# Kernel tuning notes

Measured on AMD Instinct MI355X. Metric: run time of the kernel, lower is better.

## Reference

```python
import jax, jax.numpy as jnp
import numpy as np
from jax import lax

NUM_GROUP = 128   # G
GROUP_SIZE = 32   # S
ENC = 384         # encoder_channel
BN_EPS = 1e-5


def fps(pos, K):
    # farthest point sampling; deterministic start at index 0. pos: [B,N,3] -> idx [B,K]
    B, N, _ = pos.shape
    d0 = jnp.full((B, N), jnp.inf, pos.dtype)
    start = jnp.zeros((B,), jnp.int32)

    def step(carry, _):
        d, last = carry
        p = jnp.take_along_axis(pos, last[:, None, None], axis=1)  # [B,1,3]
        dist = jnp.sum((pos - p) ** 2, -1)
        d = jnp.minimum(d, dist)
        nxt = jnp.argmax(d, axis=1).astype(jnp.int32)
        return (d, nxt), last

    _, idxs = lax.scan(step, (d0, start), None, length=K)  # [K,B]
    return jnp.transpose(idxs)


def knn_idx(q, t, k):
    # squared euclidean distances, k smallest (sorted ascending)
    d2 = (jnp.sum(q * q, -1)[:, :, None] + jnp.sum(t * t, -1)[:, None, :]
          - 2.0 * jnp.einsum('bqc,bnc->bqn', q, t))
    _, idx = lax.top_k(-d2, k)
    return idx


def gather_nn(x, idx):
    # x: [B,N,C], idx: [B,...] -> [B,...,C]
    return jax.vmap(lambda a, i: a[i])(x, idx)


def disambiguate(lps, vecs):
    # lps: [B,G,S,3], vecs: [B,G,3]; flip vec if it points away from the majority of points
    S = lps.shape[2]
    proj = jnp.einsum('bgc,bgsc->bgs', vecs, lps)
    n_pos = jnp.sum((proj > 0).astype(jnp.float32), axis=2, keepdims=True)
    flip = (n_pos < 0.5 * S).astype(jnp.float32)
    return (1.0 - 2.0 * flip) * vecs


def bn(x, g, b):
    # eval-mode BatchNorm with running_mean=0, running_var=1
    return x * (g / jnp.sqrt(1.0 + BN_EPS)) + b


def forward(pc, W1, b1, g1, be1, W2, b2, W3, b3, g2, be2, W4, b4):
    # ---- Group: FPS + KNN gather ----
    rep = fps(pc, NUM_GROUP)                      # [B,G]
    center = gather_nn(pc, rep)                   # [B,G,3]
    nn = knn_idx(center, pc, GROUP_SIZE)          # [B,G,S]
    neigh = gather_nn(pc, nn) - center[:, :, None]  # [B,G,S,3] centered local sets
    # ---- LRF: weighted PCA via 3x3 eigensolve ----
    norms = jnp.linalg.norm(neigh, axis=3, keepdims=True)
    w = jnp.max(norms, axis=2, keepdims=True) - norms
    w = w / (jnp.sum(w, axis=2, keepdims=True) + 1e-6)
    sp = 100.0 * neigh
    covs = jnp.einsum('bgsk,bgsl->bgkl', w * sp, sp)  # [B,G,3,3]
    _, eigvec = jnp.linalg.eigh(covs)                 # eigenvalues ascending
    z = disambiguate(neigh, eigvec[..., 0])           # smallest-eig axis
    x_ax = disambiguate(neigh, eigvec[..., 2])        # largest-eig axis
    y = jnp.cross(z, x_ax)
    lrfs = jnp.stack((z, y, x_ax), axis=3)            # [B,G,3,3] columns z,y,x
    rot = jnp.einsum('bgsc,bgcd->bgsd', neigh, lrfs)  # rotation-normalized points
    # ---- LocalPointSetEncoder: kernel-1 convs as matmuls ----
    f = jnp.einsum('bgsc,oc->bgso', rot, W1) + b1     # [B,G,S,128]
    f = jax.nn.relu(bn(f, g1, be1))
    f = jnp.einsum('bgso,po->bgsp', f, W2) + b2       # [B,G,S,256]
    fg = jnp.max(f, axis=2, keepdims=True)            # [B,G,1,256]
    f = jnp.concatenate([jnp.broadcast_to(fg, f.shape), f], axis=-1)  # [B,G,S,512]
    f = jnp.einsum('bgsc,oc->bgso', f, W3) + b3       # [B,G,S,512]
    f = jax.nn.relu(bn(f, g2, be2))
    f = jnp.einsum('bgso,po->bgsp', f, W4) + b4       # [B,G,S,ENC]
    return jnp.max(f, axis=2)                          # [B,G,ENC]


def setup_inputs() -> dict:
    key = jax.random.key(0)
    ks = jax.random.split(key, 6)
    B, N = 32, 8192
    w = lambda k, shape: (jax.random.normal(k, shape, jnp.float32) * 0.05)
    return {
        'pc': jax.random.normal(ks[0], (B, N, 3), jnp.float32),
        'W1': w(ks[1], (128, 3)), 'b1': jnp.zeros((128,), jnp.float32),
        'g1': jnp.ones((128,), jnp.float32), 'be1': jnp.zeros((128,), jnp.float32),
        'W2': w(ks[2], (256, 128)), 'b2': jnp.zeros((256,), jnp.float32),
        'W3': w(ks[3], (512, 512)), 'b3': jnp.zeros((512,), jnp.float32),
        'g2': jnp.ones((512,), jnp.float32), 'be2': jnp.zeros((512,), jnp.float32),
        'W4': w(ks[4], (ENC, 512)), 'b4': jnp.zeros((ENC,), jnp.float32),
    }


def reference(pc, W1, b1, g1, be1, W2, b2, W3, b3, g2, be2, W4, b4):
    return forward(pc, W1, b1, g1, be1, W2, b2, W3, b3, g2, be2, W4, b4)
```

## Files before the change

### kernel.cpp

```cpp
#include <hip/hip_runtime.h>
#include <math.h>

#define B_ 32
#define N_ 8192
#define G_ 128
#define S_ 32
#define ENC_ 384

typedef __attribute__((ext_vector_type(8))) short short8;
typedef __attribute__((ext_vector_type(4))) float f32x4;
typedef __attribute__((ext_vector_type(2))) unsigned u32x2;

__device__ __forceinline__ unsigned short f2bf(float x) {
  unsigned u = __float_as_uint(x);
  u = u + 0x7fffu + ((u >> 16) & 1u);
  return (unsigned short)(u >> 16);
}

__device__ __forceinline__ unsigned pk_bf16(float a, float b) {
  unsigned r;
  asm("v_cvt_pk_bf16_f32 %0, %1, %2" : "=v"(r) : "v"(a), "v"(b));
  return r;
}

template <int CTRL, int RM>
__device__ __forceinline__ unsigned long long dpp_max_rm(unsigned long long k) {
  const int lo = (int)(unsigned)k, hi = (int)(unsigned)(k >> 32);
  const int olo = __builtin_amdgcn_update_dpp(0, lo, CTRL, RM, 0xF, true);
  const int ohi = __builtin_amdgcn_update_dpp(0, hi, CTRL, RM, 0xF, true);
  const unsigned long long o =
      ((unsigned long long)(unsigned)ohi << 32) | (unsigned)(unsigned)olo;
  return o > k ? o : k;
}

template <int CTRL>
__device__ __forceinline__ float dpp_fmax(float v) {
  const int x = __builtin_amdgcn_update_dpp(0, __float_as_int(v), CTRL, 0xF, 0xF, true);
  return fmaxf(v, __int_as_float(x));
}
__device__ __forceinline__ float rowmax16(float v) {
  v = dpp_fmax<0x128>(v);
  v = dpp_fmax<0x124>(v);
  v = dpp_fmax<0x122>(v);
  v = dpp_fmax<0x121>(v);
  return v;
}

__global__ __launch_bounds__(512) void fps_kernel(const float* __restrict__ pc,
                                                  int* __restrict__ rep) {
  #pragma clang fp contract(off)
  extern __shared__ char smraw[];
  unsigned long long (*redbuf)[8] = (unsigned long long (*)[8])smraw;
  float* sx = (float*)(smraw + 128);
  float* sy = sx + N_;
  float* sz = sy + N_;
  const int b = blockIdx.x;
  const float* p = pc + (size_t)b * N_ * 3;
  const int tid = threadIdx.x;
  for (int i = tid; i < N_; i += 512) {
    sx[i] = p[i * 3 + 0];
    sy[i] = p[i * 3 + 1];
    sz[i] = p[i * 3 + 2];
  }
  __syncthreads();
  float X[16], Y[16], Z[16], D[16];
  #pragma unroll
  for (int j = 0; j < 16; ++j) {
    const int idx = tid + j * 512;
    X[j] = sx[idx]; Y[j] = sy[idx]; Z[j] = sz[idx];
    D[j] = INFINITY;
  }
  int last = 0;
  const int lane = tid & 63, wave = tid >> 6;
  for (int k = 0; k < G_; ++k) {
    if (tid == 0) rep[b * G_ + k] = last;
    const float px = sx[last], py = sy[last], pz = sz[last];
    float bestv = -1.0f;
    int besti = 0;
    #pragma unroll
    for (int j = 0; j < 16; ++j) {
      const float dx = X[j] - px, dy = Y[j] - py, dz = Z[j] - pz;
      float dist = dx * dx;
      dist += dy * dy;
      dist += dz * dz;
      const float dj = fminf(D[j], dist);
      D[j] = dj;
      if (dj > bestv) { bestv = dj; besti = tid + j * 512; }
    }
    unsigned long long key =
        ((unsigned long long)__float_as_uint(bestv) << 32) | (unsigned)(8191 - besti);
    key = dpp_max_rm<0xB1, 0xF>(key);
    key = dpp_max_rm<0x4E, 0xF>(key);
    key = dpp_max_rm<0x141, 0xF>(key);
    key = dpp_max_rm<0x140, 0xF>(key);
    key = dpp_max_rm<0x142, 0xA>(key);
    key = dpp_max_rm<0x143, 0xC>(key);
    const int par = k & 1;
    if (lane == 63) redbuf[par][wave] = key;
    __syncthreads();
    unsigned long long kk = redbuf[par][0];
    #pragma unroll
    for (int w = 1; w < 8; ++w) {
      const unsigned long long o = redbuf[par][w];
      if (o > kk) kk = o;
    }
    last = 8191 - (int)(kk & 0xFFFFFFFFu);
  }
}

__global__ __launch_bounds__(256) void knn_kernel(const float* __restrict__ pc,
                                                  const int* __restrict__ rep,
                                                  int* __restrict__ nn) {
  #pragma clang fp contract(off)
  const int bg = blockIdx.x;
  const int b = bg >> 7;
  const float* p = pc + (size_t)b * N_ * 3;
  const int tid = threadIdx.x;
  const int lane = tid & 63, wave = tid >> 6;
  const int ridx = rep[bg];
  const float qx = p[ridx * 3 + 0], qy = p[ridx * 3 + 1], qz = p[ridx * 3 + 2];
  float nq = qx * qx;
  nq += qy * qy;
  nq += qz * qz;
  unsigned ub[32];
  #pragma unroll
  for (int j = 0; j < 32; ++j) {
    const int idx = tid + j * 256;
    const float tx = p[idx * 3 + 0], ty = p[idx * 3 + 1], tz = p[idx * 3 + 2];
    float nt = tx * tx;
    nt += ty * ty;
    nt += tz * tz;
    float dt = qx * tx;
    dt += qy * ty;
    dt += qz * tz;
    const float d2 = (nq + nt) - 2.0f * dt;
    unsigned u = __float_as_uint(d2);
    u = (u & 0x80000000u) ? ~u : (u | 0x80000000u);
    ub[j] = u;
  }

  __shared__ unsigned hist[256];
  __shared__ unsigned wsum[4];
  __shared__ int s_bin, s_cexc, s_hbin, s_cnt;
  __shared__ unsigned long long keys[32];

  unsigned long long curPrefix = 0;
  int need = 32;
  int prevShift = 45;
  int stopShift = 0;
  unsigned long long stopPrefix = 0;
  const int shifts[6] = {37, 29, 21, 13, 5, 0};
  #pragma unroll 1
  for (int pass = 0; pass < 6; ++pass) {
    const int sh = shifts[pass];
    const int width = prevShift - sh;
    const unsigned msk = (1u << width) - 1u;
    hist[tid] = 0;
    if (pass == 0 && tid == 0) s_cnt = 0;
    __syncthreads();
    #pragma unroll
    for (int j = 0; j < 32; ++j) {
      const unsigned long long key =
          ((unsigned long long)ub[j] << 13) | (unsigned)(tid + j * 256);
      if ((key >> prevShift) == curPrefix)
        atomicAdd(&hist[(unsigned)(key >> sh) & msk], 1u);
    }
    __syncthreads();
    const unsigned v = hist[tid];
    unsigned c = v;
    #pragma unroll
    for (int off = 1; off <= 32; off <<= 1) {
      const unsigned o = __shfl_up(c, (unsigned)off);
      if (lane >= off) c += o;
    }
    if (lane == 63) wsum[wave] = c;
    __syncthreads();
    unsigned pre = 0;
    if (wave > 0) pre += wsum[0];
    if (wave > 1) pre += wsum[1];
    if (wave > 2) pre += wsum[2];
    const unsigned cine = c + pre;
    const unsigned cexc = cine - v;
    if (cexc < (unsigned)need && (unsigned)need <= cine) {
      s_bin = tid;
      s_cexc = (int)cexc;
      s_hbin = (int)v;
    }
    __syncthreads();
    curPrefix = (curPrefix << width) | (unsigned)s_bin;
    need -= s_cexc;
    prevShift = sh;
    if (need == s_hbin) {
      stopShift = sh;
      stopPrefix = curPrefix;
      break;
    }
  }
  #pragma unroll
  for (int j = 0; j < 32; ++j) {
    const unsigned long long key =
        ((unsigned long long)ub[j] << 13) | (unsigned)(tid + j * 256);
    if ((key >> stopShift) <= stopPrefix) {
      const int pos = atomicAdd(&s_cnt, 1);
      keys[pos] = key;
    }
  }
  __syncthreads();
  if (tid < 32) {
    const unsigned long long kt = keys[tid];
    int rank = 0;
    #pragma unroll
    for (int j = 0; j < 32; ++j) rank += (keys[j] < kt) ? 1 : 0;
    nn[bg * S_ + rank] = (int)(kt & 8191u);
  }
}

__device__ __forceinline__ double slapy2d(double x, double y) {
  return sqrt(x * x + y * y);
}

__device__ void slartg_(double f, double g, double& c, double& s, double& r) {
  if (g == 0.0) { c = 1.0; s = 0.0; r = f; }
  else if (f == 0.0) { c = 0.0; s = copysign(1.0, g); r = fabs(g); }
  else {
    const double d = sqrt(f * f + g * g);
    c = fabs(f) / d;
    r = copysign(d, f);
    s = g / r;
  }
}

__device__ void slaev2_(double a, double b, double c, double& rt1, double& rt2,
                        double& cs1, double& sn1) {
  const double sm = a + c, df = a - c;
  const double adf = fabs(df), tb = b + b, ab = fabs(tb);
  double acmx, acmn;
  if (fabs(a) > fabs(c)) { acmx = a; acmn = c; } else { acmx = c; acmn = a; }
  double rt;
  if (adf > ab) rt = adf * sqrt(1.0 + (ab / adf) * (ab / adf));
  else if (adf < ab) rt = ab * sqrt(1.0 + (adf / ab) * (adf / ab));
  else rt = ab * sqrt(2.0);
  int sgn1;
  if (sm < 0.0) { rt1 = 0.5 * (sm - rt); sgn1 = -1; rt2 = (acmx / rt1) * acmn - (b / rt1) * b; }
  else if (sm > 0.0) { rt1 = 0.5 * (sm + rt); sgn1 = 1; rt2 = (acmx / rt1) * acmn - (b / rt1) * b; }
  else { rt1 = 0.5 * rt; rt2 = -0.5 * rt; sgn1 = 1; }
  double cs;
  int sgn2;
  if (df >= 0.0) { cs = df + rt; sgn2 = 1; } else { cs = df - rt; sgn2 = -1; }
  const double acs = fabs(cs);
  if (acs > ab) {
    const double ct = -tb / cs;
    sn1 = 1.0 / sqrt(1.0 + ct * ct);
    cs1 = ct * sn1;
  } else {
    if (ab == 0.0) { cs1 = 1.0; sn1 = 0.0; }
    else {
      const double tn = -cs / tb;
      cs1 = 1.0 / sqrt(1.0 + tn * tn);
      sn1 = tn * cs1;
    }
  }
  if (sgn1 == sgn2) { const double tn = cs1; cs1 = -sn1; sn1 = tn; }
}

__device__ void eigh33_lapack(const double A[3][3], double dout[3], double Zo[3][3]) {
  double d[3], e[2];
  double Z[3][3];
  {
    const double a00 = A[0][0], a10 = A[1][0], a20 = A[2][0];
    const double a11 = A[1][1], a21 = A[2][1], a22 = A[2][2];
    if (fabs(a20) == 0.0) {
      d[0] = a00; d[1] = a11; d[2] = a22; e[0] = a10; e[1] = a21;
      Z[0][0] = 1; Z[0][1] = 0; Z[0][2] = 0;
      Z[1][0] = 0; Z[1][1] = 1; Z[1][2] = 0;
      Z[2][0] = 0; Z[2][1] = 0; Z[2][2] = 1;
    } else {
      const double beta = -copysign(slapy2d(a10, a20), a10);
      const double tau = (beta - a10) / beta;
      const double v2 = a20 / (a10 - beta);
      const double h11 = 1.0 - tau;
      const double h12 = -tau * v2;
      const double h22 = 1.0 - tau * v2 * v2;
      const double m10 = h11 * a10 + h12 * a20;
      const double m11 = h11 * a11 + h12 * a21;
      const double m12 = h11 * a21 + h12 * a22;
      const double m21 = h12 * a11 + h22 * a21;
      const double m22 = h12 * a21 + h22 * a22;
      d[0] = a00;
      d[1] = m11 * h11 + m12 * h12;
      d[2] = m21 * h12 + m22 * h22;
      e[0] = m10;
      e[1] = m21 * h11 + m22 * h12;
      Z[0][0] = 1; Z[0][1] = 0;   Z[0][2] = 0;
      Z[1][0] = 0; Z[1][1] = h11; Z[1][2] = h12;
      Z[2][0] = 0; Z[2][1] = h12; Z[2][2] = h22;
    }
  }
  const double eps = 5.9604644775390625e-08;
  const double eps2 = eps * eps;
  const double safmin = 1.1754943508222875e-38;
  int jtot = 0;
  const int nmaxit = 90;
  int l1 = 0;
  while (l1 <= 2) {
    if (l1 > 0) e[l1 - 1] = 0.0;
    int m;
    for (m = l1; m <= 1; ++m) {
      const double tst = fabs(e[m]);
      if (tst == 0.0) break;
      if (tst <= (sqrt(fabs(d[m])) * sqrt(fabs(d[m + 1]))) * eps) { e[m] = 0.0; break; }
    }
    int l = l1;
    const int lsv = l;
    int lend = m;
    const int lendsv = lend;
    l1 = m + 1;
    if (lend == l) continue;
    if (fabs(d[lend]) < fabs(d[l])) { lend = lsv; l = lendsv; }
    if (lend > l) {
      for (;;) {
        int mq;
        for (mq = l; mq <= lend - 1; ++mq) {
          const double tst = e[mq] * e[mq];
          if (tst <= (eps2 * fabs(d[mq])) * fabs(d[mq + 1]) + safmin) break;
        }
        if (mq < lend) e[mq] = 0.0;
        double p = d[l];
        if (mq == l) { d[l] = p; l = l + 1; if (l <= lend) continue; break; }
        if (mq == l + 1) {
          double rt1, rt2, c, s;
          slaev2_(d[l], e[l], d[l + 1], rt1, rt2, c, s);
          for (int i = 0; i < 3; ++i) {
            const double t1 = Z[i][l + 1], t0 = Z[i][l];
            Z[i][l + 1] = c * t1 - s * t0;
            Z[i][l] = s * t1 + c * t0;
          }
          d[l] = rt1; d[l + 1] = rt2; e[l] = 0.0;
          l += 2;
          if (l <= lend) continue;
          break;
        }
        if (jtot == nmaxit) break;
        ++jtot;
        double g = (d[l + 1] - p) / (2.0 * e[l]);
        double r = slapy2d(g, 1.0);
        g = d[mq] - p + e[l] / (g + copysign(r, g));
        double s = 1.0, c = 1.0;
        p = 0.0;
        double csv[2], ssv[2];
        for (int i = mq - 1; i >= l; --i) {
          const double f = s * e[i];
          const double bb = c * e[i];
          slartg_(g, f, c, s, r);
          if (i != mq - 1) e[i + 1] = r;
          g = d[i + 1] - p;
          r = (d[i] - g) * s + 2.0 * c * bb;
          p = s * r;
          d[i + 1] = g + p;
          g = c * r - bb;
          csv[i] = c; ssv[i] = -s;
        }
        const int mm = mq - l + 1;
        for (int j = mm - 2; j >= 0; --j) {
          const double ct = csv[l + j], st = ssv[l + j];
          for (int i = 0; i < 3; ++i) {
            const double t1 = Z[i][l + j + 1];
            Z[i][l + j + 1] = ct * t1 - st * Z[i][l + j];
            Z[i][l + j] = st * t1 + ct * Z[i][l + j];
          }
        }
        d[l] = d[l] - p;
        e[l] = g;
      }
    } else {
      for (;;) {
        int mq;
        for (mq = l; mq >= lend + 1; --mq) {
          const double tst = e[mq - 1] * e[mq - 1];
          if (tst <= (eps2 * fabs(d[mq])) * fabs(d[mq - 1]) + safmin) break;
        }
        if (mq > lend) e[mq - 1] = 0.0;
        double p = d[l];
        if (mq == l) { d[l] = p; l = l - 1; if (l >= lend) continue; break; }
        if (mq == l - 1) {
          double rt1, rt2, c, s;
          slaev2_(d[l - 1], e[l - 1], d[l], rt1, rt2, c, s);
          for (int i = 0; i < 3; ++i) {
            const double t1 = Z[i][l], t0 = Z[i][l - 1];
            Z[i][l] = c * t1 - s * t0;
            Z[i][l - 1] = s * t1 + c * t0;
          }
          d[l - 1] = rt1; d[l] = rt2; e[l - 1] = 0.0;
          l -= 2;
          if (l >= lend) continue;
          break;
        }
        if (jtot == nmaxit) break;
        ++jtot;
        double g = (d[l - 1] - p) / (2.0 * e[l - 1]);
        double r = slapy2d(g, 1.0);
        g = d[mq] - p + e[l - 1] / (g + copysign(r, g));
        double s = 1.0, c = 1.0;
        p = 0.0;
        double csv[2], ssv[2];
        for (int i = mq; i <= l - 1; ++i) {
          const double f = s * e[i];
          const double bb = c * e[i];
          slartg_(g, f, c, s, r);
          if (i != mq) e[i - 1] = r;
          g = d[i] - p;
          r = (d[i + 1] - g) * s + 2.0 * c * bb;
          p = s * r;
          d[i] = g + p;
          g = c * r - bb;
          csv[i] = c; ssv[i] = s;
        }
        const int mm = l - mq + 1;
        for (int j = 0; j <= mm - 2; ++j) {
          const double ct = csv[mq + j], st = ssv[mq + j];
          for (int i = 0; i < 3; ++i) {
            const double t1 = Z[i][mq + j + 1];
            Z[i][mq + j + 1] = ct * t1 - st * Z[i][mq + j];
            Z[i][mq + j] = st * t1 + ct * Z[i][mq + j];
          }
        }
        d[l] = d[l] - p;
        e[l - 1] = g;
      }
    }
  }
  for (int ii = 1; ii < 3; ++ii) {
    const int i = ii - 1;
    int k = i;
    double p = d[i];
    for (int j = ii; j < 3; ++j)
      if (d[j] < p) { k = j; p = d[j]; }
    if (k != i) {
      d[k] = d[i];
      d[i] = p;
      for (int q = 0; q < 3; ++q) {
        const double t = Z[q][i];
        Z[q][i] = Z[q][k];
        Z[q][k] = t;
      }
    }
  }
  dout[0] = d[0]; dout[1] = d[1]; dout[2] = d[2];
  for (int i = 0; i < 3; ++i)
    for (int j = 0; j < 3; ++j) Zo[i][j] = Z[i][j];
}

__global__ __launch_bounds__(64) void lrf_kernel(const float* __restrict__ pc,
                                                 const int* __restrict__ rep,
                                                 const int* __restrict__ nn,
                                                 float* __restrict__ rot) {
  #pragma clang fp contract(off)
  const int bg = blockIdx.x;
  const int b = bg >> 7;
  const float* p = pc + (size_t)b * N_ * 3;
  const int lane = threadIdx.x;
  const int s = lane & 31;
  const int ridx = rep[bg];
  const float cx = p[ridx * 3 + 0], cy = p[ridx * 3 + 1], cz = p[ridx * 3 + 2];
  const int idx = nn[bg * S_ + s];
  const float nx = p[idx * 3 + 0] - cx;
  const float ny = p[idx * 3 + 1] - cy;
  const float nz = p[idx * 3 + 2] - cz;
  float nrm2 = nx * nx;
  nrm2 += ny * ny;
  nrm2 += nz * nz;
  const float nrm = sqrtf(nrm2);
  float wmax = nrm;
  #pragma unroll
  for (int off = 16; off >= 1; off >>= 1) wmax = fmaxf(wmax, __shfl_xor(wmax, off));
  float w = wmax - nrm;
  float wsum = w;
  #pragma unroll
  for (int off = 16; off >= 1; off >>= 1) wsum += __shfl_xor(wsum, off);
  w = w / (wsum + 1e-6f);
  const float spx = 100.0f * nx, spy = 100.0f * ny, spz = 100.0f * nz;
  const float wx = w * spx, wy = w * spy, wz = w * spz;
  float c00 = wx * spx, c01 = wx * spy, c02 = wx * spz;
  float c11 = wy * spy, c12 = wy * spz, c22 = wz * spz;
  #pragma unroll
  for (int off = 16; off >= 1; off >>= 1) {
    c00 += __shfl_xor(c00, off); c01 += __shfl_xor(c01, off); c02 += __shfl_xor(c02, off);
    c11 += __shfl_xor(c11, off); c12 += __shfl_xor(c12, off); c22 += __shfl_xor(c22, off);
  }
  double A[3][3] = {{(double)c00, (double)c01, (double)c02},
                    {(double)c01, (double)c11, (double)c12},
                    {(double)c02, (double)c12, (double)c22}};
  double lam[3], Zm[3][3];
  eigh33_lapack(A, lam, Zm);
  float zx = (float)Zm[0][0], zy = (float)Zm[1][0], zz = (float)Zm[2][0];
  float xx = (float)Zm[0][2], xy = (float)Zm[1][2], xz = (float)Zm[2][2];
  float pj = zx * nx;
  pj += zy * ny;
  pj += zz * nz;
  int npos = __popcll(__ballot(pj > 0.0f) & 0xFFFFFFFFull);
  if (npos < 16) { zx = -zx; zy = -zy; zz = -zz; }
  pj = xx * nx;
  pj += xy * ny;
  pj += xz * nz;
  npos = __popcll(__ballot(pj > 0.0f) & 0xFFFFFFFFull);
  if (npos < 16) { xx = -xx; xy = -xy; xz = -xz; }
  const float yx = zy * xz - zz * xy;
  const float yy = zz * xx - zx * xz;
  const float yz = zx * xy - zy * xx;
  if (lane < 32) {
    float r0 = nx * zx; r0 += ny * zy; r0 += nz * zz;
    float r1 = nx * yx; r1 += ny * yy; r1 += nz * yz;
    float r2 = nx * xx; r2 += ny * xy; r2 += nz * xz;
    const size_t base = (size_t)(bg * S_ + s) * 3;
    rot[base + 0] = r0;
    rot[base + 1] = r1;
    rot[base + 2] = r2;
  }
}

#define P2_ 4096
#define P3_ 16384
#define P4_ 24576
__global__ __launch_bounds__(256) void convw_kernel(
    const float* __restrict__ W2, const float* __restrict__ W3,
    const float* __restrict__ W4, short* __restrict__ w2t,
    short* __restrict__ w3gt, short* __restrict__ w3ft,
    short* __restrict__ w4t) {
  int t = blockIdx.x * 256 + threadIdx.x;
  const float* src;
  short* dst;
  if (t < P2_) {
    const int lane = t & 63, kt = (t >> 6) & 3, nt = t >> 8;
    src = W2 + (nt * 16 + (lane & 15)) * 128 + kt * 32 + ((lane >> 4) << 3);
    dst = w2t + t * 8;
  } else if (t < P2_ + P3_) {
    const int p = t - P2_;
    const int lane = p & 63, kt = (p >> 6) & 7, nt = p >> 9;
    src = W3 + (nt * 16 + (lane & 15)) * 512 + kt * 32 + ((lane >> 4) << 3);
    dst = w3gt + p * 8;
  } else if (t < P2_ + 2 * P3_) {
    const int p = t - P2_ - P3_;
    const int lane = p & 63, kt = (p >> 6) & 7, nt = p >> 9;
    src = W3 + (nt * 16 + (lane & 15)) * 512 + 256 + kt * 32 + ((lane >> 4) << 3);
    dst = w3ft + p * 8;
  } else if (t < P2_ + 2 * P3_ + P4_) {
    const int p = t - P2_ - 2 * P3_;
    const int lane = p & 63, kt = (p >> 6) & 15, nt = p >> 10;
    src = W4 + (nt * 16 + (lane & 15)) * 512 + kt * 32 + ((lane >> 4) << 3);
    dst = w4t + p * 8;
  } else {
    return;
  }
  short8 v;
  #pragma unroll
  for (int j = 0; j < 8; ++j) v[j] = (short)f2bf(src[j]);
  *(short8*)dst = v;
}

#define OFF_A3   0
#define OFF_R1   32768
#define OFF_FGA  65536
#define OFF_BASE 73728
#define OFF_SROT 77824
#define LDS_MLP  78592

__device__ __forceinline__ int swz(int row, int byteoff) {
  return byteoff ^ ((row & 7) << 4);
}

__global__ __launch_bounds__(512) void mlp_kernel(
    const float* __restrict__ rot,
    const float* __restrict__ W1, const float* __restrict__ b1,
    const float* __restrict__ g1, const float* __restrict__ be1,
    const float* __restrict__ b2, const float* __restrict__ b3,
    const float* __restrict__ g2, const float* __restrict__ be2,
    const float* __restrict__ b4,
    const short* __restrict__ w2t, const short* __restrict__ w3gt,
    const short* __restrict__ w3ft, const short* __restrict__ w4t,
    float* __restrict__ out) {
  extern __shared__ char sm[];
  const int tid = threadIdx.x;
  const int lane = tid & 63, wave = tid >> 6;
  const int l15 = lane & 15, lq = lane >> 4;
  const int bg0 = blockIdx.x * 2;
  const float inv_s = 1.0f / sqrtf(1.0f + 1e-5f);

  if (tid < 192) ((float*)(sm + OFF_SROT))[tid] = rot[(size_t)bg0 * 96 + tid];
  for (int i = tid; i < 2048; i += 512) ((int*)(sm + OFF_FGA))[i] = 0;
  __syncthreads();

  {
    const int o2 = (tid & 63) * 2;
    const int rbase = tid >> 6;
    const float w00 = W1[o2 * 3], w01 = W1[o2 * 3 + 1], w02 = W1[o2 * 3 + 2];
    const float w10 = W1[o2 * 3 + 3], w11 = W1[o2 * 3 + 4], w12 = W1[o2 * 3 + 5];
    const float b10 = b1[o2], b11 = b1[o2 + 1];
    const float sc0 = g1[o2] * inv_s, sc1 = g1[o2 + 1] * inv_s;
    const float sh0 = be1[o2], sh1 = be1[o2 + 1];
    const float* sr = (const float*)(sm + OFF_SROT);
    #pragma unroll
    for (int t = 0; t < 8; ++t) {
      const int row = rbase + t * 8;
      const float x = sr[row * 3], y = sr[row * 3 + 1], z = sr[row * 3 + 2];
      const float v0 = fmaxf((x * w00 + y * w01 + z * w02 + b10) * sc0 + sh0, 0.0f);
      const float v1 = fmaxf((x * w10 + y * w11 + z * w12 + b11) * sc1 + sh1, 0.0f);
      *(unsigned*)(sm + OFF_R1 + swz(row, row * 256 + o2 * 2)) = pk_bf16(v0, v1);
    }
  }
  __syncthreads();

  {
    f32x4 acc[2][4];
    #pragma unroll
    for (int j = 0; j < 2; ++j)
      #pragma unroll
      for (int st = 0; st < 4; ++st) acc[j][st] = (f32x4){0.f, 0.f, 0.f, 0.f};
    #pragma unroll 1
    for (int kt = 0; kt < 4; ++kt) {
      short8 bf[4];
      #pragma unroll
      for (int st = 0; st < 4; ++st) {
        const int s = st * 16 + l15;
        bf[st] = *(const short8*)(sm + OFF_R1 + swz(s, s * 256 + kt * 64 + (lq << 4)));
      }
      #pragma unroll
      for (int j = 0; j < 2; ++j) {
        const short8 wa = *(const short8*)(w2t + (((wave * 2 + j) * 4 + kt) * 64 + lane) * 8);
        #pragma unroll
        for (int st = 0; st < 4; ++st)
          acc[j][st] = __builtin_amdgcn_mfma_f32_16x16x32_bf16(wa, bf[st], acc[j][st], 0, 0, 0);
      }
    }
    #pragma unroll
    for (int j = 0; j < 2; ++j) {
      const int n0 = (wave * 2 + j) * 16 + (lq << 2);
      const f32x4 b2v = *(const f32x4*)(b2 + n0);
      float vv[4][4];
      #pragma unroll
      for (int st = 0; st < 4; ++st) {
        #pragma unroll
        for (int r = 0; r < 4; ++r) vv[st][r] = acc[j][st][r] + b2v[r];
        const int s = st * 16 + l15;
        const unsigned lo = pk_bf16(vv[st][0], vv[st][1]);
        const unsigned hi = pk_bf16(vv[st][2], vv[st][3]);
        *(u32x2*)(sm + OFF_A3 + swz(s, s * 512 + n0 * 2)) = (u32x2){lo, hi};
      }
      float fg0[4], fg1[4];
      #pragma unroll
      for (int r = 0; r < 4; ++r) {
        fg0[r] = rowmax16(fmaxf(vv[0][r], vv[1][r]));
        fg1[r] = rowmax16(fmaxf(vv[2][r], vv[3][r]));
      }
      if (l15 == 0) {
        *(u32x2*)(sm + OFF_FGA + swz(0, n0 * 2)) =
            (u32x2){pk_bf16(fg0[0], fg0[1]), pk_bf16(fg0[2], fg0[3])};
      } else if (l15 == 1) {
        *(u32x2*)(sm + OFF_FGA + swz(1, 512 + n0 * 2)) =
            (u32x2){pk_bf16(fg1[0], fg1[1]), pk_bf16(fg1[2], fg1[3])};
      }
    }
  }
  __syncthreads();

  {
    f32x4 acg[4];
    #pragma unroll
    for (int q = 0; q < 4; ++q) acg[q] = (f32x4){0.f, 0.f, 0.f, 0.f};
    #pragma unroll 1
    for (int kt = 0; kt < 8; ++kt) {
      const short8 bf = *(const short8*)(sm + OFF_FGA + swz(l15, l15 * 512 + kt * 64 + (lq << 4)));
      #pragma unroll
      for (int q = 0; q < 4; ++q) {
        const short8 wa = *(const short8*)(w3gt + (((wave * 4 + q) * 8 + kt) * 64 + lane) * 8);
        acg[q] = __builtin_amdgcn_mfma_f32_16x16x32_bf16(wa, bf, acg[q], 0, 0, 0);
      }
    }
    if (l15 < 2) {
      #pragma unroll
      for (int q = 0; q < 4; ++q) {
        const int n3 = (wave * 4 + q) * 16 + (lq << 2);
        const f32x4 b3v = *(const f32x4*)(b3 + n3);
        *(f32x4*)(sm + OFF_BASE + l15 * 2048 + n3 * 4) = acg[q] + b3v;
      }
    }
  }
  __syncthreads();

  f32x4 acc4[3][4];
  #pragma unroll
  for (int q = 0; q < 3; ++q)
    #pragma unroll
    for (int st = 0; st < 4; ++st) acc4[q][st] = (f32x4){0.f, 0.f, 0.f, 0.f};

  #pragma unroll 1
  for (int p = 0; p < 2; ++p) {
    {
      f32x4 ac[2][4];
      #pragma unroll
      for (int jj = 0; jj < 2; ++jj)
        #pragma unroll
        for (int st = 0; st < 4; ++st) ac[jj][st] = (f32x4){0.f, 0.f, 0.f, 0.f};
      #pragma unroll 1
      for (int kt = 0; kt < 8; ++kt) {
        short8 bf[4];
        #pragma unroll
        for (int st = 0; st < 4; ++st) {
          const int s = st * 16 + l15;
          bf[st] = *(const short8*)(sm + OFF_A3 + swz(s, s * 512 + kt * 64 + (lq << 4)));
        }
        #pragma unroll
        for (int jj = 0; jj < 2; ++jj) {
          const int mt = p * 16 + wave * 2 + jj;
          const short8 wa = *(const short8*)(w3ft + ((mt * 8 + kt) * 64 + lane) * 8);
          #pragma unroll
          for (int st = 0; st < 4; ++st)
            ac[jj][st] = __builtin_amdgcn_mfma_f32_16x16x32_bf16(wa, bf[st], ac[jj][st], 0, 0, 0);
        }
      }
      #pragma unroll
      for (int jj = 0; jj < 2; ++jj) {
        const int ng = (p * 16 + wave * 2 + jj) * 16 + (lq << 2);
        const int nl = (wave * 2 + jj) * 16 + (lq << 2);
        f32x4 scv = *(const f32x4*)(g2 + ng);
        const f32x4 shv = *(const f32x4*)(be2 + ng);
        #pragma unroll
        for (int r = 0; r < 4; ++r) scv[r] *= inv_s;
        #pragma unroll
        for (int st = 0; st < 4; ++st) {
          const int g = st >> 1;
          const f32x4 bsv = *(const f32x4*)(sm + OFF_BASE + g * 2048 + ng * 4);
          float v[4];
          #pragma unroll
          for (int r = 0; r < 4; ++r)
            v[r] = fmaxf((ac[jj][st][r] + bsv[r]) * scv[r] + shv[r], 0.0f);
          const int s = st * 16 + l15;
          *(u32x2*)(sm + OFF_R1 + swz(s, s * 512 + nl * 2)) =
              (u32x2){pk_bf16(v[0], v[1]), pk_bf16(v[2], v[3])};
        }
      }
    }
    __syncthreads();
    #pragma unroll 1
    for (int ktl = 0; ktl < 8; ++ktl) {
      short8 bf[4];
      #pragma unroll
      for (int st = 0; st < 4; ++st) {
        const int s = st * 16 + l15;
        bf[st] = *(const short8*)(sm + OFF_R1 + swz(s, s * 512 + ktl * 64 + (lq << 4)));
      }
      #pragma unroll
      for (int q = 0; q < 3; ++q) {
        const short8 wa =
            *(const short8*)(w4t + ((((wave * 3 + q) * 16) + p * 8 + ktl) * 64 + lane) * 8);
        #pragma unroll
        for (int st = 0; st < 4; ++st)
          acc4[q][st] = __builtin_amdgcn_mfma_f32_16x16x32_bf16(wa, bf[st], acc4[q][st], 0, 0, 0);
      }
    }
    __syncthreads();
  }

  #pragma unroll
  for (int q = 0; q < 3; ++q) {
    const int n4 = (wave * 3 + q) * 16 + (lq << 2);
    const f32x4 b4v = *(const f32x4*)(b4 + n4);
    float m0[4], m1[4];
    #pragma unroll
    for (int r = 0; r < 4; ++r) {
      m0[r] = rowmax16(fmaxf(acc4[q][0][r], acc4[q][1][r]));
      m1[r] = rowmax16(fmaxf(acc4[q][2][r], acc4[q][3][r]));
    }
    if (l15 == 0) {
      f32x4 o;
      #pragma unroll
      for (int r = 0; r < 4; ++r) o[r] = m0[r] + b4v[r];
      *(f32x4*)(out + (size_t)bg0 * ENC_ + n4) = o;
    } else if (l15 == 1) {
      f32x4 o;
      #pragma unroll
      for (int r = 0; r < 4; ++r) o[r] = m1[r] + b4v[r];
      *(f32x4*)(out + (size_t)(bg0 + 1) * ENC_ + n4) = o;
    }
  }
}

extern "C" void kernel_launch(void* const* d_in, const int* in_sizes, int n_in,
                              void* d_out, int out_size, void* d_ws, size_t ws_size,
                              hipStream_t stream) {
  const float* pc  = (const float*)d_in[0];
  const float* W1  = (const float*)d_in[1];
  const float* b1  = (const float*)d_in[2];
  const float* g1  = (const float*)d_in[3];
  const float* be1 = (const float*)d_in[4];
  const float* W2  = (const float*)d_in[5];
  const float* b2  = (const float*)d_in[6];
  const float* W3  = (const float*)d_in[7];
  const float* b3  = (const float*)d_in[8];
  const float* g2  = (const float*)d_in[9];
  const float* be2 = (const float*)d_in[10];
  const float* W4  = (const float*)d_in[11];
  const float* b4  = (const float*)d_in[12];
  float* out = (float*)d_out;
  char* ws = (char*)d_ws;
  int* rep    = (int*)ws;
  int* nn     = (int*)(ws + 16384);
  float* rot  = (float*)(ws + 540672);
  short* w2t  = (short*)(ws + 2113536);
  short* w3gt = (short*)(ws + 2179072);
  short* w3ft = (short*)(ws + 2441216);
  short* w4t  = (short*)(ws + 2703360);

  const size_t fps_lds = 128 + (size_t)3 * N_ * 4;

  convw_kernel<<<240, 256, 0, stream>>>(W2, W3, W4, w2t, w3gt, w3ft, w4t);
  fps_kernel<<<B_, 512, fps_lds, stream>>>(pc, rep);
  knn_kernel<<<B_ * G_, 256, 0, stream>>>(pc, rep, nn);
  lrf_kernel<<<B_ * G_, 64, 0, stream>>>(pc, rep, nn, rot);
  mlp_kernel<<<B_ * G_ / 2, 512, LDS_MLP, stream>>>(
      rot, W1, b1, g1, be1, b2, b3, g2, be2, b4, w2t, w3gt, w3ft, w4t, out);
}
```

Baseline: 401.3 us.

## Speed up KNN radix select with per-wave histograms and early candidate cutoff

The radix-select top-k in the KNN kernel now keeps a separate shared-memory histogram per wave to reduce atomic contention, and uses 32-bit comparisons on the distance bits for passes whose shift leaves the index bits untouched. The refinement loop stops as soon as the candidate set fits in 128 entries rather than requiring an exact 32-element boundary, and a small rank sort over those candidates writes out the 32 nearest. This cuts histogram passes and 64-bit work, at the cost of a larger final ranking step and non-unrolled loops.

Result: no change. 396.7 us (-1.1%).

```diff
diff --git a/kernel.cpp b/kernel.cpp
--- a/kernel.cpp
+++ b/kernel.cpp
@@ -139,10 +139,10 @@
     ub[j] = u;
   }
 
-  __shared__ unsigned hist[256];
+  __shared__ unsigned hist[4][256];
   __shared__ unsigned wsum[4];
   __shared__ int s_bin, s_cexc, s_hbin, s_cnt;
-  __shared__ unsigned long long keys[32];
+  __shared__ unsigned long long cand[128];
 
   unsigned long long curPrefix = 0;
   int need = 32;
@@ -155,18 +155,30 @@
     const int sh = shifts[pass];
     const int width = prevShift - sh;
     const unsigned msk = (1u << width) - 1u;
-    hist[tid] = 0;
+    #pragma unroll
+    for (int w = 0; w < 4; ++w) hist[w][tid] = 0;
     if (pass == 0 && tid == 0) s_cnt = 0;
     __syncthreads();
-    #pragma unroll
-    for (int j = 0; j < 32; ++j) {
-      const unsigned long long key =
-          ((unsigned long long)ub[j] << 13) | (unsigned)(tid + j * 256);
-      if ((key >> prevShift) == curPrefix)
-        atomicAdd(&hist[(unsigned)(key >> sh) & msk], 1u);
+    if (sh >= 13) {
+      const int shp = prevShift - 13, shd = sh - 13;
+      const unsigned pref32 = (unsigned)curPrefix;
+      #pragma unroll 1
+      for (int j = 0; j < 32; ++j) {
+        const unsigned u = ub[j];
+        if ((shp >= 32 ? 0u : (u >> shp)) == pref32)
+          atomicAdd(&hist[wave][(u >> shd) & msk], 1u);
+      }
+    } else {
+      #pragma unroll 1
+      for (int j = 0; j < 32; ++j) {
+        const unsigned long long key =
+            ((unsigned long long)ub[j] << 13) | (unsigned)(tid + j * 256);
+        if ((key >> prevShift) == curPrefix)
+          atomicAdd(&hist[wave][(unsigned)(key >> sh) & msk], 1u);
+      }
     }
     __syncthreads();
-    const unsigned v = hist[tid];
+    const unsigned v = hist[0][tid] + hist[1][tid] + hist[2][tid] + hist[3][tid];
     unsigned c = v;
     #pragma unroll
     for (int off = 1; off <= 32; off <<= 1) {
@@ -190,28 +202,41 @@
     curPrefix = (curPrefix << width) | (unsigned)s_bin;
     need -= s_cexc;
     prevShift = sh;
-    if (need == s_hbin) {
+    if ((32 - need) + s_hbin <= 128) {
       stopShift = sh;
       stopPrefix = curPrefix;
       break;
     }
   }
-  #pragma unroll
-  for (int j = 0; j < 32; ++j) {
-    const unsigned long long key =
-        ((unsigned long long)ub[j] << 13) | (unsigned)(tid + j * 256);
-    if ((key >> stopShift) <= stopPrefix) {
-      const int pos = atomicAdd(&s_cnt, 1);
-      keys[pos] = key;
+  if (stopShift >= 13) {
+    const int shd = stopShift - 13;
+    const unsigned pref32 = (unsigned)stopPrefix;
+    #pragma unroll 1
+    for (int j = 0; j < 32; ++j) {
+      if ((ub[j] >> shd) <= pref32) {
+        const int pos = atomicAdd(&s_cnt, 1);
+        cand[pos] = ((unsigned long long)ub[j] << 13) | (unsigned)(tid + j * 256);
+      }
+    }
+  } else {
+    #pragma unroll 1
+    for (int j = 0; j < 32; ++j) {
+      const unsigned long long key =
+          ((unsigned long long)ub[j] << 13) | (unsigned)(tid + j * 256);
+      if ((key >> stopShift) <= stopPrefix) {
+        const int pos = atomicAdd(&s_cnt, 1);
+        cand[pos] = key;
+      }
     }
   }
   __syncthreads();
-  if (tid < 32) {
-    const unsigned long long kt = keys[tid];
+  const int cnt = s_cnt;
+  if (tid < cnt) {
+    const unsigned long long kt = cand[tid];
     int rank = 0;
-    #pragma unroll
-    for (int j = 0; j < 32; ++j) rank += (keys[j] < kt) ? 1 : 0;
-    nn[bg * S_ + rank] = (int)(kt & 8191u);
+    #pragma unroll 1
+    for (int j = 0; j < cnt; ++j) rank += (cand[j] < kt) ? 1 : 0;
+    if (rank < 32) nn[bg * S_ + rank] = (int)(kt & 8191u);
   }
 }
 
```
